# Kernel optimization log

Hardware: AMD Instinct MI355X
Metric: run time of the kernel (lower is better)

Reference implementation:

```python
import jax, jax.numpy as jnp
import numpy as np

N = 50000   # nodes (cells)
E = 800000  # directed edges
D = 512     # input/output feature dim (genes)
H = D // 64 # bottleneck dim = 8
LN_EPS = 1e-5


def setup_inputs() -> dict:
    key = jax.random.key(0)
    ks = jax.random.split(key, 6)
    x = jax.random.normal(ks[0], (N, D), dtype=jnp.float32)
    edge_index = jax.random.randint(ks[1], (2, E), 0, N, dtype=jnp.int64)
    size_factors = jax.random.uniform(ks[2], (N, 1), dtype=jnp.float32) + 0.5
    s1 = float(1.0 / np.sqrt(D))
    W1 = jax.random.uniform(ks[3], (D, H), jnp.float32, -s1, s1)
    b1 = jnp.zeros((H,), jnp.float32)
    gamma = jnp.ones((H,), jnp.float32)
    beta = jnp.zeros((H,), jnp.float32)
    s2 = float(1.0 / np.sqrt(H))
    W2 = jax.random.uniform(ks[4], (H, D), jnp.float32, -s2, s2)
    b2 = jnp.zeros((D,), jnp.float32)
    return {"x": x, "size_factors": size_factors, "W1": W1, "b1": b1,
            "gamma": gamma, "beta": beta, "W2": W2, "b2": b2,
            "edge_index": edge_index}


def _gcn_conv(x, W, b, src, dst, norm):
    # PyG GCNConv: linear transform, then sym-normalized scatter-add aggregation.
    h = x @ W                                   # [N, out]
    msg = h[src] * norm[:, None]                # [E+N, out] gather + scale
    out = jax.ops.segment_sum(msg, dst, num_segments=N)  # scatter-add
    return out + b


def reference(x, size_factors, W1, b1, gamma, beta, W2, b2, edge_index):
    loops = jnp.arange(N, dtype=edge_index.dtype)
    src = jnp.concatenate([edge_index[0], loops])  # add self-loops
    dst = jnp.concatenate([edge_index[1], loops])
    deg = jax.ops.segment_sum(jnp.ones_like(src, dtype=x.dtype), dst,
                              num_segments=N)       # deg >= 1 via self-loops
    dinv = jax.lax.rsqrt(deg)
    norm = dinv[src] * dinv[dst]                    # [E+N]

    h = _gcn_conv(x, W1, b1, src, dst, norm)        # [N, H]
    mu = jnp.mean(h, axis=-1, keepdims=True)
    var = jnp.var(h, axis=-1, keepdims=True)
    h = (h - mu) * jax.lax.rsqrt(var + LN_EPS) * gamma + beta
    h = jax.nn.relu(h)
    # dropout p=0.0 -> identity
    out = jax.nn.relu(_gcn_conv(h, W2, b2, src, dst, norm))  # [N, D]
    return out * size_factors
```

## Files before the change

kernel.cpp:

```cpp
#include <hip/hip_runtime.h>

#define NN 50000
#define EE 800000
#define DD 512
#define HH 8
#define BA 160
#define CHUNK 5000
#define NBIN 196
#define BCAP 4608
#define GBLK 782
#define NTILE 3125
#define AGBLK 1563
#define SCANT 192

typedef short bf16x8 __attribute__((ext_vector_type(8)));
typedef float f32x4 __attribute__((ext_vector_type(4)));

union U16 { uint4 u; bf16x8 v; unsigned short h[8]; };

__device__ __forceinline__ unsigned short f2bf(float f) {
    union { float f; unsigned int i; } c; c.f = f;
    unsigned int i = c.i;
    i += 0x7fffu + ((i >> 16) & 1u);
    return (unsigned short)(i >> 16);
}

__global__ __launch_bounds__(256) void k_gemm1_hist(const float4* __restrict__ x4,
                                                    const float* __restrict__ W1,
                                                    const int* __restrict__ dst,
                                                    float* __restrict__ t1,
                                                    int* __restrict__ blockhist) {
    __shared__ int smem[4096];
    int t = threadIdx.x;
    if (blockIdx.x >= GBLK) {
        int blk = blockIdx.x - GBLK;
        int* h = smem;
        h[t] = 0; __syncthreads();
        int base = blk * CHUNK;
#pragma unroll
        for (int it = 0; it < 20; ++it) {
            int i = it * 256 + t;
            if (i < CHUNK) atomicAdd(&h[dst[base + i] >> 8], 1);
        }
        __syncthreads();
        blockhist[blk * 256 + t] = h[t];
        return;
    }
    unsigned short* sbf = (unsigned short*)smem;
    for (int i = t; i < 16 * 64 * 8; i += 256) {
        int lane = (i >> 3) & 63, j = i & 7;
        int n = lane & 15;
        int k = (i >> 9) * 32 + ((lane >> 4) * 8) + j;
        sbf[i] = (n < HH) ? f2bf(W1[k * HH + n]) : (unsigned short)0;
    }
    __syncthreads();
    int wave = t >> 6, lane = t & 63;
    int tile = blockIdx.x * 4 + wave;
    if (tile >= NTILE) return;
    int node0 = tile * 16;
    int m = lane & 15, q = lane >> 4;
    const float4* xrow = x4 + (size_t)(node0 + m) * (DD / 4) + q * 2;
    const uint4* bfrag = (const uint4*)sbf;
    f32x4 acc = {0.f, 0.f, 0.f, 0.f};

    float4 bufA[8], bufB[8];
#define LOADG(buf, g)                                                      \
    _Pragma("unroll")                                                      \
    for (int s = 0; s < 4; ++s) {                                          \
        buf[2 * s]     = xrow[((g) * 4 + s) * 8];                          \
        buf[2 * s + 1] = xrow[((g) * 4 + s) * 8 + 1];                      \
    }
#define MFMAG(buf, g)                                                      \
    _Pragma("unroll")                                                      \
    for (int s = 0; s < 4; ++s) {                                          \
        U16 a, b;                                                          \
        float4 u0 = buf[2 * s], u1 = buf[2 * s + 1];                       \
        a.h[0] = f2bf(u0.x); a.h[1] = f2bf(u0.y);                          \
        a.h[2] = f2bf(u0.z); a.h[3] = f2bf(u0.w);                          \
        a.h[4] = f2bf(u1.x); a.h[5] = f2bf(u1.y);                          \
        a.h[6] = f2bf(u1.z); a.h[7] = f2bf(u1.w);                          \
        b.u = bfrag[((g) * 4 + s) * 64 + lane];                            \
        acc = __builtin_amdgcn_mfma_f32_16x16x32_bf16(a.v, b.v, acc, 0, 0, 0); \
    }
    LOADG(bufA, 0)
    LOADG(bufB, 1)
    MFMAG(bufA, 0)
    LOADG(bufA, 2)
    MFMAG(bufB, 1)
    LOADG(bufB, 3)
    MFMAG(bufA, 2)
    MFMAG(bufB, 3)
#undef LOADG
#undef MFMAG
    if (m < HH) {
        int base = (node0 + q * 4) * HH + m;
        t1[base]          = acc[0];
        t1[base + HH]     = acc[1];
        t1[base + 2 * HH] = acc[2];
        t1[base + 3 * HH] = acc[3];
    }
}

__global__ __launch_bounds__(SCANT) void k_scan_a(int* __restrict__ blockhist,
                                                  int* __restrict__ binTotal) {
    __shared__ int s[SCANT];
    int bin = blockIdx.x, t = threadIdx.x;
    int v = (t < BA) ? blockhist[t * 256 + bin] : 0;
    s[t] = v; __syncthreads();
    for (int off = 1; off < SCANT; off <<= 1) {
        int x = (t >= off) ? s[t - off] : 0;
        __syncthreads();
        if (t >= off) s[t] += x;
        __syncthreads();
    }
    if (t < BA) blockhist[t * 256 + bin] = s[t] - v;
    if (t == SCANT - 1) binTotal[bin] = s[t];
}

__global__ __launch_bounds__(256) void k_scan_b(const int* __restrict__ binTotal,
                                                int* __restrict__ binBase,
                                                int* __restrict__ row) {
    __shared__ int s[256];
    int t = threadIdx.x;
    int v = binTotal[t];
    s[t] = v; __syncthreads();
    for (int off = 1; off < 256; off <<= 1) {
        int x = (t >= off) ? s[t - off] : 0;
        __syncthreads();
        if (t >= off) s[t] += x;
        __syncthreads();
    }
    binBase[t] = s[t] - v;
    if (t == 255) { binBase[256] = s[255]; row[NN] = s[255]; }
}

__global__ __launch_bounds__(256) void k_scatter(const int* __restrict__ eidx,
                                                 const int* __restrict__ blockhist,
                                                 const int* __restrict__ binBase,
                                                 int* __restrict__ bucket) {
    __shared__ int cur[256];
    int t = threadIdx.x, blk = blockIdx.x;
    cur[t] = binBase[t] + blockhist[blk * 256 + t]; __syncthreads();
    int base = blk * CHUNK;
#pragma unroll
    for (int it = 0; it < 20; ++it) {
        int i = it * 256 + t;
        if (i < CHUNK) {
            int s = eidx[base + i], d = eidx[EE + base + i];
            int pos = atomicAdd(&cur[d >> 8], 1);
            bucket[pos] = (s << 8) | (d & 255);
        }
    }
}

__global__ __launch_bounds__(256) void k_build(const int* __restrict__ bucket,
                                               const int* __restrict__ binBase,
                                               int* __restrict__ row,
                                               int* __restrict__ adj,
                                               float* __restrict__ dinvA,
                                               float* __restrict__ t1) {
    __shared__ int smem[2 * BCAP + 768];
    int t = threadIdx.x;
    int bin = blockIdx.x;
    int n0 = bin << 8;
    int segStart = binBase[bin];
    int count = binBase[bin + 1] - segStart;
    if (count > BCAP) count = BCAP;
    int* lds_in  = smem;
    int* lds_out = smem + BCAP;
    int* cnt     = smem + 2 * BCAP;
    int* off     = smem + 2 * BCAP + 256;
    int* cur2    = smem + 2 * BCAP + 512;
    cnt[t] = 0; __syncthreads();
    for (int i = t; i < count; i += 256) {
        int p = bucket[segStart + i];
        lds_in[i] = p;
        atomicAdd(&cnt[p & 255], 1);
    }
    __syncthreads();
    off[t] = cnt[t]; __syncthreads();
    for (int o = 1; o < 256; o <<= 1) {
        int x = (t >= o) ? off[t - o] : 0;
        __syncthreads();
        if (t >= o) off[t] += x;
        __syncthreads();
    }
    int excl = off[t] - cnt[t];
    cur2[t] = excl;
    int n = n0 + t;
    if (n < NN) {
        row[n] = segStart + excl;
        float dv = rsqrtf((float)cnt[t] + 1.0f);
        dinvA[n] = dv;
        float4* tp = (float4*)(t1 + (size_t)n * HH);
        float4 a = tp[0], b = tp[1];
        a.x *= dv; a.y *= dv; a.z *= dv; a.w *= dv;
        b.x *= dv; b.y *= dv; b.z *= dv; b.w *= dv;
        tp[0] = a; tp[1] = b;
    }
    __syncthreads();
    for (int i = t; i < count; i += 256) {
        int p = lds_in[i];
        int pos = atomicAdd(&cur2[p & 255], 1);
        lds_out[pos] = p >> 8;
    }
    __syncthreads();
    for (int i = t; i < count; i += 256)
        adj[segStart + i] = lds_out[i];
}

__global__ __launch_bounds__(256) void k_agg1(const float* __restrict__ t1,
                                              const int* __restrict__ row,
                                              const int* __restrict__ adj,
                                              const float* __restrict__ dinvA,
                                              const float* __restrict__ b1,
                                              const float* __restrict__ gma,
                                              const float* __restrict__ bta,
                                              float* __restrict__ h2) {
    int gid = blockIdx.x * 256 + threadIdx.x;
    int n = gid >> 3, f = gid & 7;
    if (n >= NN) return;
    int beg = row[n], end = row[n + 1];
    float dv = dinvA[n];
    float acc = t1[(size_t)n * HH + f];
    int i = beg;
    for (; i < end && (i & 3); ++i)
        acc += t1[(size_t)adj[i] * HH + f];
    const int4* a4 = (const int4*)adj;
    for (; i + 8 <= end; i += 8) {
        int4 e0 = a4[i >> 2], e1 = a4[(i >> 2) + 1];
        float v0 = t1[(size_t)e0.x * HH + f], v1 = t1[(size_t)e0.y * HH + f];
        float v2 = t1[(size_t)e0.z * HH + f], v3 = t1[(size_t)e0.w * HH + f];
        float v4 = t1[(size_t)e1.x * HH + f], v5 = t1[(size_t)e1.y * HH + f];
        float v6 = t1[(size_t)e1.z * HH + f], v7 = t1[(size_t)e1.w * HH + f];
        acc += ((v0 + v1) + (v2 + v3)) + ((v4 + v5) + (v6 + v7));
    }
    if (i + 4 <= end) {
        int4 e0 = a4[i >> 2];
        float v0 = t1[(size_t)e0.x * HH + f], v1 = t1[(size_t)e0.y * HH + f];
        float v2 = t1[(size_t)e0.z * HH + f], v3 = t1[(size_t)e0.w * HH + f];
        acc += (v0 + v1) + (v2 + v3);
        i += 4;
    }
    for (; i < end; ++i)
        acc += t1[(size_t)adj[i] * HH + f];
    acc = acc * dv + b1[f];
    float s = acc;
    s += __shfl_xor(s, 1); s += __shfl_xor(s, 2); s += __shfl_xor(s, 4);
    float mu = s * 0.125f;
    float dx = acc - mu;
    float sq = dx * dx;
    sq += __shfl_xor(sq, 1); sq += __shfl_xor(sq, 2); sq += __shfl_xor(sq, 4);
    float rs = rsqrtf(sq * 0.125f + 1e-5f);
    h2[(size_t)n * HH + f] = fmaxf(dx * rs * gma[f] + bta[f], 0.f) * dv;
}

__global__ __launch_bounds__(256) void k_agg2_gemm2(const float* __restrict__ h2,
                                                    const int* __restrict__ row,
                                                    const int* __restrict__ adj,
                                                    const float* __restrict__ dinvA,
                                                    const float* __restrict__ W2,
                                                    const float* __restrict__ b2,
                                                    const float* __restrict__ sf,
                                                    float* __restrict__ out) {
    __shared__ float sA[32 * 8];
    int tid = threadIdx.x;
    int c = tid & 63, g = tid >> 6, d0 = c * 8;
    float w[8][8];
#pragma unroll
    for (int k = 0; k < 8; ++k) {
        float4 u0 = *(const float4*)(W2 + k * DD + d0);
        float4 u1 = *(const float4*)(W2 + k * DD + d0 + 4);
        w[k][0] = u0.x; w[k][1] = u0.y; w[k][2] = u0.z; w[k][3] = u0.w;
        w[k][4] = u1.x; w[k][5] = u1.y; w[k][6] = u1.z; w[k][7] = u1.w;
    }
    float bb[8];
    {
        float4 u0 = *(const float4*)(b2 + d0);
        float4 u1 = *(const float4*)(b2 + d0 + 4);
        bb[0] = u0.x; bb[1] = u0.y; bb[2] = u0.z; bb[3] = u0.w;
        bb[4] = u1.x; bb[5] = u1.y; bb[6] = u1.z; bb[7] = u1.w;
    }
    int nl = tid >> 3, f = tid & 7;
    int n = blockIdx.x * 32 + nl;
    if (n < NN) {
        int beg = row[n], end = row[n + 1];
        float dv = dinvA[n];
        float acc = h2[(size_t)n * HH + f];
        int i = beg;
        for (; i < end && (i & 3); ++i)
            acc += h2[(size_t)adj[i] * HH + f];
        const int4* a4 = (const int4*)adj;
        for (; i + 8 <= end; i += 8) {
            int4 e0 = a4[i >> 2], e1 = a4[(i >> 2) + 1];
            float v0 = h2[(size_t)e0.x * HH + f], v1 = h2[(size_t)e0.y * HH + f];
            float v2 = h2[(size_t)e0.z * HH + f], v3 = h2[(size_t)e0.w * HH + f];
            float v4 = h2[(size_t)e1.x * HH + f], v5 = h2[(size_t)e1.y * HH + f];
            float v6 = h2[(size_t)e1.z * HH + f], v7 = h2[(size_t)e1.w * HH + f];
            acc += ((v0 + v1) + (v2 + v3)) + ((v4 + v5) + (v6 + v7));
        }
        if (i + 4 <= end) {
            int4 e0 = a4[i >> 2];
            float v0 = h2[(size_t)e0.x * HH + f], v1 = h2[(size_t)e0.y * HH + f];
            float v2 = h2[(size_t)e0.z * HH + f], v3 = h2[(size_t)e0.w * HH + f];
            acc += (v0 + v1) + (v2 + v3);
            i += 4;
        }
        for (; i < end; ++i)
            acc += h2[(size_t)adj[i] * HH + f];
        sA[nl * 8 + f] = acc * dv;
    }
    __syncthreads();
#pragma unroll
    for (int i = 0; i < 8; ++i) {
        int rrow = i * 4 + g;
        int n2 = blockIdx.x * 32 + rrow;
        if (n2 < NN) {
            float a[8];
#pragma unroll
            for (int j = 0; j < 8; ++j) a[j] = sA[rrow * 8 + j];
            float s = sf[n2];
            float acc[8];
#pragma unroll
            for (int j = 0; j < 8; ++j) acc[j] = bb[j];
#pragma unroll
            for (int k = 0; k < 8; ++k)
#pragma unroll
                for (int j = 0; j < 8; ++j) acc[j] += a[k] * w[k][j];
            float4 o0 = make_float4(fmaxf(acc[0], 0.f) * s, fmaxf(acc[1], 0.f) * s,
                                    fmaxf(acc[2], 0.f) * s, fmaxf(acc[3], 0.f) * s);
            float4 o1 = make_float4(fmaxf(acc[4], 0.f) * s, fmaxf(acc[5], 0.f) * s,
                                    fmaxf(acc[6], 0.f) * s, fmaxf(acc[7], 0.f) * s);
            float4* op = (float4*)(out + (size_t)n2 * DD + d0);
            op[0] = o0;
            op[1] = o1;
        }
    }
}

extern "C" void kernel_launch(void* const* d_in, const int* in_sizes, int n_in,
                              void* d_out, int out_size, void* d_ws, size_t ws_size,
                              hipStream_t stream) {
    (void)in_sizes; (void)n_in; (void)out_size; (void)ws_size;
    const float* x   = (const float*)d_in[0];
    const float* sf  = (const float*)d_in[1];
    const float* W1  = (const float*)d_in[2];
    const float* b1  = (const float*)d_in[3];
    const float* gma = (const float*)d_in[4];
    const float* bta = (const float*)d_in[5];
    const float* W2  = (const float*)d_in[6];
    const float* b2  = (const float*)d_in[7];
    const int* eidx  = (const int*)d_in[8];
    float* out = (float*)d_out;

    char* ws = (char*)d_ws;
    int*   blockhist = (int*)(ws + 0);
    int*   binBase   = (int*)(ws + 262144);
    int*   binTotal  = (int*)(ws + 262144 + 2048);
    int*   row       = (int*)(ws + (1 << 20));
    float* dinvA     = (float*)(ws + 2 * (1 << 20));
    float* t1        = (float*)(ws + 3 * (1 << 20));
    float* h2        = (float*)(ws + 5 * (1 << 20));
    int*   adj       = (int*)(ws + 7 * (1 << 20));
    int*   bucket    = (int*)(ws + 11 * (1 << 20));

    k_gemm1_hist<<<GBLK + BA, 256, 0, stream>>>((const float4*)x, W1, eidx + EE,
                                                t1, blockhist);
    k_scan_a<<<256, SCANT, 0, stream>>>(blockhist, binTotal);
    k_scan_b<<<1, 256, 0, stream>>>(binTotal, binBase, row);
    k_scatter<<<BA, 256, 0, stream>>>(eidx, blockhist, binBase, bucket);
    k_build<<<NBIN, 256, 0, stream>>>(bucket, binBase, row, adj, dinvA, t1);
    k_agg1<<<AGBLK, 256, 0, stream>>>(t1, row, adj, dinvA, b1, gma, bta, h2);
    k_agg2_gemm2<<<AGBLK, 256, 0, stream>>>(h2, row, adj, dinvA, W2, b2, sf, out);
}
```

Before: 270.9 us.

## Replace binned two-level CSR build with global-atomic degree count and fill

Swaps the bucketed CSR construction (per-block histograms, two scans, bucket scatter, LDS-local sort) for a simpler scheme: global atomic degree counting, a two-kernel prefix scan over nodes, and a fill kernel that places each edge with a global atomicAdd on a per-node cursor. The aim is to remove the bucket pass and the heavier LDS build kernel, cutting one round trip of edge data. In exchange it relies on scattered global atomics, and the neighbour order within each row becomes nondeterministic, which can change float summation order. It also adds a memset launch.

New measurement: 316.6 us. +16.9%, slower.

```diff
diff --git a/kernel.cpp b/kernel.cpp
--- a/kernel.cpp
+++ b/kernel.cpp
@@ -4,14 +4,12 @@
 #define EE 800000
 #define DD 512
 #define HH 8
-#define BA 160
-#define CHUNK 5000
-#define NBIN 196
-#define BCAP 4608
 #define GBLK 782
+#define DBLK 391
 #define NTILE 3125
 #define AGBLK 1563
-#define SCANT 192
+#define SB 196
+#define NPAD 50176
 
 typedef short bf16x8 __attribute__((ext_vector_type(8)));
 typedef float f32x4 __attribute__((ext_vector_type(4)));
@@ -25,25 +23,20 @@
     return (unsigned short)(i >> 16);
 }
 
-__global__ __launch_bounds__(256) void k_gemm1_hist(const float4* __restrict__ x4,
-                                                    const float* __restrict__ W1,
-                                                    const int* __restrict__ dst,
-                                                    float* __restrict__ t1,
-                                                    int* __restrict__ blockhist) {
+__global__ __launch_bounds__(256) void k_gemm1_deg(const float4* __restrict__ x4,
+                                                   const float* __restrict__ W1,
+                                                   const int* __restrict__ dst,
+                                                   float* __restrict__ t1,
+                                                   int* __restrict__ deg) {
     __shared__ int smem[4096];
     int t = threadIdx.x;
     if (blockIdx.x >= GBLK) {
-        int blk = blockIdx.x - GBLK;
-        int* h = smem;
-        h[t] = 0; __syncthreads();
-        int base = blk * CHUNK;
-#pragma unroll
-        for (int it = 0; it < 20; ++it) {
-            int i = it * 256 + t;
-            if (i < CHUNK) atomicAdd(&h[dst[base + i] >> 8], 1);
+        int base = (blockIdx.x - GBLK) * 2048;
+#pragma unroll
+        for (int it = 0; it < 8; ++it) {
+            int i = base + it * 256 + t;
+            if (i < EE) atomicAdd(&deg[dst[i]], 1);
         }
-        __syncthreads();
-        blockhist[blk * 256 + t] = h[t];
         return;
     }
     unsigned short* sbf = (unsigned short*)smem;
@@ -101,28 +94,13 @@
     }
 }
 
-__global__ __launch_bounds__(SCANT) void k_scan_a(int* __restrict__ blockhist,
-                                                  int* __restrict__ binTotal) {
-    __shared__ int s[SCANT];
-    int bin = blockIdx.x, t = threadIdx.x;
-    int v = (t < BA) ? blockhist[t * 256 + bin] : 0;
-    s[t] = v; __syncthreads();
-    for (int off = 1; off < SCANT; off <<= 1) {
-        int x = (t >= off) ? s[t - off] : 0;
-        __syncthreads();
-        if (t >= off) s[t] += x;
-        __syncthreads();
-    }
-    if (t < BA) blockhist[t * 256 + bin] = s[t] - v;
-    if (t == SCANT - 1) binTotal[bin] = s[t];
-}
-
-__global__ __launch_bounds__(256) void k_scan_b(const int* __restrict__ binTotal,
-                                                int* __restrict__ binBase,
-                                                int* __restrict__ row) {
+__global__ __launch_bounds__(256) void k_scanA(const int* __restrict__ deg,
+                                               int* __restrict__ dlocal,
+                                               int* __restrict__ bsum) {
     __shared__ int s[256];
-    int t = threadIdx.x;
-    int v = binTotal[t];
+    int b = blockIdx.x, t = threadIdx.x;
+    int n = b * 256 + t;
+    int v = deg[n];
     s[t] = v; __syncthreads();
     for (int off = 1; off < 256; off <<= 1) {
         int x = (t >= off) ? s[t - off] : 0;
@@ -130,83 +108,51 @@
         if (t >= off) s[t] += x;
         __syncthreads();
     }
-    binBase[t] = s[t] - v;
-    if (t == 255) { binBase[256] = s[255]; row[NN] = s[255]; }
-}
-
-__global__ __launch_bounds__(256) void k_scatter(const int* __restrict__ eidx,
-                                                 const int* __restrict__ blockhist,
-                                                 const int* __restrict__ binBase,
-                                                 int* __restrict__ bucket) {
-    __shared__ int cur[256];
-    int t = threadIdx.x, blk = blockIdx.x;
-    cur[t] = binBase[t] + blockhist[blk * 256 + t]; __syncthreads();
-    int base = blk * CHUNK;
-#pragma unroll
-    for (int it = 0; it < 20; ++it) {
-        int i = it * 256 + t;
-        if (i < CHUNK) {
-            int s = eidx[base + i], d = eidx[EE + base + i];
-            int pos = atomicAdd(&cur[d >> 8], 1);
-            bucket[pos] = (s << 8) | (d & 255);
-        }
-    }
-}
-
-__global__ __launch_bounds__(256) void k_build(const int* __restrict__ bucket,
-                                               const int* __restrict__ binBase,
+    dlocal[n] = s[t] - v;
+    if (t == 255) bsum[b] = s[255];
+}
+
+__global__ __launch_bounds__(256) void k_scanB(const int* __restrict__ deg,
+                                               const int* __restrict__ dlocal,
+                                               const int* __restrict__ bsum,
+                                               float* __restrict__ t1,
                                                int* __restrict__ row,
-                                               int* __restrict__ adj,
-                                               float* __restrict__ dinvA,
-                                               float* __restrict__ t1) {
-    __shared__ int smem[2 * BCAP + 768];
-    int t = threadIdx.x;
-    int bin = blockIdx.x;
-    int n0 = bin << 8;
-    int segStart = binBase[bin];
-    int count = binBase[bin + 1] - segStart;
-    if (count > BCAP) count = BCAP;
-    int* lds_in  = smem;
-    int* lds_out = smem + BCAP;
-    int* cnt     = smem + 2 * BCAP;
-    int* off     = smem + 2 * BCAP + 256;
-    int* cur2    = smem + 2 * BCAP + 512;
-    cnt[t] = 0; __syncthreads();
-    for (int i = t; i < count; i += 256) {
-        int p = bucket[segStart + i];
-        lds_in[i] = p;
-        atomicAdd(&cnt[p & 255], 1);
-    }
+                                               int* __restrict__ cur,
+                                               float* __restrict__ dinvA) {
+    __shared__ int s[256];
+    int b = blockIdx.x, t = threadIdx.x;
+    s[t] = (t < SB) ? bsum[t] : 0;
     __syncthreads();
-    off[t] = cnt[t]; __syncthreads();
-    for (int o = 1; o < 256; o <<= 1) {
-        int x = (t >= o) ? off[t - o] : 0;
+    for (int off = 1; off < 256; off <<= 1) {
+        int x = (t >= off) ? s[t - off] : 0;
         __syncthreads();
-        if (t >= o) off[t] += x;
+        if (t >= off) s[t] += x;
         __syncthreads();
     }
-    int excl = off[t] - cnt[t];
-    cur2[t] = excl;
-    int n = n0 + t;
+    int base = s[b] - bsum[b];
+    int n = b * 256 + t;
     if (n < NN) {
-        row[n] = segStart + excl;
-        float dv = rsqrtf((float)cnt[t] + 1.0f);
+        int r = base + dlocal[n];
+        row[n] = r;
+        cur[n] = r;
+        float dv = rsqrtf((float)deg[n] + 1.0f);
         dinvA[n] = dv;
         float4* tp = (float4*)(t1 + (size_t)n * HH);
-        float4 a = tp[0], b = tp[1];
+        float4 a = tp[0], c = tp[1];
         a.x *= dv; a.y *= dv; a.z *= dv; a.w *= dv;
-        b.x *= dv; b.y *= dv; b.z *= dv; b.w *= dv;
-        tp[0] = a; tp[1] = b;
-    }
-    __syncthreads();
-    for (int i = t; i < count; i += 256) {
-        int p = lds_in[i];
-        int pos = atomicAdd(&cur2[p & 255], 1);
-        lds_out[pos] = p >> 8;
-    }
-    __syncthreads();
-    for (int i = t; i < count; i += 256)
-        adj[segStart + i] = lds_out[i];
+        c.x *= dv; c.y *= dv; c.z *= dv; c.w *= dv;
+        tp[0] = a; tp[1] = c;
+    }
+    if (b == 0 && t == 0) row[NN] = EE;
+}
+
+__global__ __launch_bounds__(256) void k_fill(const int* __restrict__ eidx,
+                                              int* __restrict__ cur,
+                                              int* __restrict__ adj) {
+    int i = blockIdx.x * 256 + threadIdx.x;
+    int s = eidx[i], d = eidx[EE + i];
+    int pos = atomicAdd(&cur[d], 1);
+    adj[pos] = s;
 }
 
 __global__ __launch_bounds__(256) void k_agg1(const float* __restrict__ t1,
@@ -354,22 +300,22 @@
     float* out = (float*)d_out;
 
     char* ws = (char*)d_ws;
-    int*   blockhist = (int*)(ws + 0);
-    int*   binBase   = (int*)(ws + 262144);
-    int*   binTotal  = (int*)(ws + 262144 + 2048);
-    int*   row       = (int*)(ws + (1 << 20));
-    float* dinvA     = (float*)(ws + 2 * (1 << 20));
-    float* t1        = (float*)(ws + 3 * (1 << 20));
-    float* h2        = (float*)(ws + 5 * (1 << 20));
-    int*   adj       = (int*)(ws + 7 * (1 << 20));
-    int*   bucket    = (int*)(ws + 11 * (1 << 20));
-
-    k_gemm1_hist<<<GBLK + BA, 256, 0, stream>>>((const float4*)x, W1, eidx + EE,
-                                                t1, blockhist);
-    k_scan_a<<<256, SCANT, 0, stream>>>(blockhist, binTotal);
-    k_scan_b<<<1, 256, 0, stream>>>(binTotal, binBase, row);
-    k_scatter<<<BA, 256, 0, stream>>>(eidx, blockhist, binBase, bucket);
-    k_build<<<NBIN, 256, 0, stream>>>(bucket, binBase, row, adj, dinvA, t1);
+    int*   deg    = (int*)(ws + 0);
+    int*   dlocal = (int*)(ws + 0x40000);
+    int*   bsum   = (int*)(ws + 0x80000);
+    int*   row    = (int*)(ws + (1 << 20));
+    int*   cur    = (int*)(ws + 0x180000);
+    float* dinvA  = (float*)(ws + 2 * (1 << 20));
+    float* t1     = (float*)(ws + 3 * (1 << 20));
+    float* h2     = (float*)(ws + 5 * (1 << 20));
+    int*   adj    = (int*)(ws + 7 * (1 << 20));
+
+    hipMemsetAsync(deg, 0, NPAD * sizeof(int), stream);
+    k_gemm1_deg<<<GBLK + DBLK, 256, 0, stream>>>((const float4*)x, W1, eidx + EE,
+                                                 t1, deg);
+    k_scanA<<<SB, 256, 0, stream>>>(deg, dlocal, bsum);
+    k_scanB<<<SB, 256, 0, stream>>>(deg, dlocal, bsum, t1, row, cur, dinvA);
+    k_fill<<<NTILE, 256, 0, stream>>>(eidx, cur, adj);
     k_agg1<<<AGBLK, 256, 0, stream>>>(t1, row, adj, dinvA, b1, gma, bta, h2);
     k_agg2_gemm2<<<AGBLK, 256, 0, stream>>>(h2, row, adj, dinvA, W2, b2, sf, out);
 }
```

## Pad CSR rows to multiples of four with a zero sentinel node

Applied to the files above, without the earlier changes.

Each node's adjacency list is padded to a multiple of 4 and aligned, and the padding slots point at a sentinel row N whose features are zeroed in t1 and h2. The aggregation loops then use only aligned int4 loads, with no scalar head or tail loops, and read separate begin/end arrays. This removes divergent scalar edge iterations in both aggregation kernels. The cost is extra gathers of the zero row, slightly more LDS in the build kernel, and a larger adjacency array.

Result: no change. 266.6 us (-1.6%).

```diff
diff --git a/kernel.cpp b/kernel.cpp
--- a/kernel.cpp
+++ b/kernel.cpp
@@ -8,6 +8,7 @@
 #define CHUNK 5000
 #define NBIN 196
 #define BCAP 4608
+#define BPAD 5632
 #define GBLK 782
 #define NTILE 3125
 #define AGBLK 1563
@@ -119,7 +120,7 @@
 
 __global__ __launch_bounds__(256) void k_scan_b(const int* __restrict__ binTotal,
                                                 int* __restrict__ binBase,
-                                                int* __restrict__ row) {
+                                                float* __restrict__ t1) {
     __shared__ int s[256];
     int t = threadIdx.x;
     int v = binTotal[t];
@@ -131,7 +132,8 @@
         __syncthreads();
     }
     binBase[t] = s[t] - v;
-    if (t == 255) { binBase[256] = s[255]; row[NN] = s[255]; }
+    if (t == 255) binBase[256] = s[255];
+    if (t < HH) t1[(size_t)NN * HH + t] = 0.f;
 }
 
 __global__ __launch_bounds__(256) void k_scatter(const int* __restrict__ eidx,
@@ -155,11 +157,12 @@
 
 __global__ __launch_bounds__(256) void k_build(const int* __restrict__ bucket,
                                                const int* __restrict__ binBase,
-                                               int* __restrict__ row,
+                                               int* __restrict__ beg,
+                                               int* __restrict__ endp,
                                                int* __restrict__ adj,
                                                float* __restrict__ dinvA,
                                                float* __restrict__ t1) {
-    __shared__ int smem[2 * BCAP + 768];
+    __shared__ int smem[BCAP + BPAD + 768];
     int t = threadIdx.x;
     int bin = blockIdx.x;
     int n0 = bin << 8;
@@ -168,9 +171,9 @@
     if (count > BCAP) count = BCAP;
     int* lds_in  = smem;
     int* lds_out = smem + BCAP;
-    int* cnt     = smem + 2 * BCAP;
-    int* off     = smem + 2 * BCAP + 256;
-    int* cur2    = smem + 2 * BCAP + 512;
+    int* cnt     = smem + BCAP + BPAD;
+    int* off     = smem + BCAP + BPAD + 256;
+    int* cur2    = smem + BCAP + BPAD + 512;
     cnt[t] = 0; __syncthreads();
     for (int i = t; i < count; i += 256) {
         int p = bucket[segStart + i];
@@ -178,18 +181,21 @@
         atomicAdd(&cnt[p & 255], 1);
     }
     __syncthreads();
-    off[t] = cnt[t]; __syncthreads();
+    int pcnt = (cnt[t] + 3) & ~3;
+    off[t] = pcnt; __syncthreads();
     for (int o = 1; o < 256; o <<= 1) {
         int x = (t >= o) ? off[t - o] : 0;
         __syncthreads();
         if (t >= o) off[t] += x;
         __syncthreads();
     }
-    int excl = off[t] - cnt[t];
-    cur2[t] = excl;
+    int pexcl = off[t] - pcnt;
+    cur2[t] = pexcl;
+    int pbase = ((segStart + 3) & ~3) + bin * 1024;
     int n = n0 + t;
     if (n < NN) {
-        row[n] = segStart + excl;
+        beg[n]  = pbase + pexcl;
+        endp[n] = pbase + pexcl + pcnt;
         float dv = rsqrtf((float)cnt[t] + 1.0f);
         dinvA[n] = dv;
         float4* tp = (float4*)(t1 + (size_t)n * HH);
@@ -199,35 +205,39 @@
         tp[0] = a; tp[1] = b;
     }
     __syncthreads();
+    int paddedCount = off[255];
+    for (int i = t; i < paddedCount; i += 256)
+        lds_out[i] = NN;
+    __syncthreads();
     for (int i = t; i < count; i += 256) {
         int p = lds_in[i];
         int pos = atomicAdd(&cur2[p & 255], 1);
         lds_out[pos] = p >> 8;
     }
     __syncthreads();
-    for (int i = t; i < count; i += 256)
-        adj[segStart + i] = lds_out[i];
+    for (int i = t; i < paddedCount; i += 256)
+        adj[pbase + i] = lds_out[i];
 }
 
 __global__ __launch_bounds__(256) void k_agg1(const float* __restrict__ t1,
-                                              const int* __restrict__ row,
-                                              const int* __restrict__ adj,
+                                              const int* __restrict__ beg,
+                                              const int* __restrict__ endp,
                                               const float* __restrict__ dinvA,
                                               const float* __restrict__ b1,
                                               const float* __restrict__ gma,
                                               const float* __restrict__ bta,
+                                              const int* __restrict__ adj,
                                               float* __restrict__ h2) {
+    if (blockIdx.x == 0 && threadIdx.x < HH)
+        h2[(size_t)NN * HH + threadIdx.x] = 0.f;
     int gid = blockIdx.x * 256 + threadIdx.x;
     int n = gid >> 3, f = gid & 7;
     if (n >= NN) return;
-    int beg = row[n], end = row[n + 1];
+    int i = beg[n], e = endp[n];
     float dv = dinvA[n];
     float acc = t1[(size_t)n * HH + f];
-    int i = beg;
-    for (; i < end && (i & 3); ++i)
-        acc += t1[(size_t)adj[i] * HH + f];
     const int4* a4 = (const int4*)adj;
-    for (; i + 8 <= end; i += 8) {
+    for (; i + 8 <= e; i += 8) {
         int4 e0 = a4[i >> 2], e1 = a4[(i >> 2) + 1];
         float v0 = t1[(size_t)e0.x * HH + f], v1 = t1[(size_t)e0.y * HH + f];
         float v2 = t1[(size_t)e0.z * HH + f], v3 = t1[(size_t)e0.w * HH + f];
@@ -235,15 +245,12 @@
         float v6 = t1[(size_t)e1.z * HH + f], v7 = t1[(size_t)e1.w * HH + f];
         acc += ((v0 + v1) + (v2 + v3)) + ((v4 + v5) + (v6 + v7));
     }
-    if (i + 4 <= end) {
+    if (i < e) {
         int4 e0 = a4[i >> 2];
         float v0 = t1[(size_t)e0.x * HH + f], v1 = t1[(size_t)e0.y * HH + f];
         float v2 = t1[(size_t)e0.z * HH + f], v3 = t1[(size_t)e0.w * HH + f];
         acc += (v0 + v1) + (v2 + v3);
-        i += 4;
-    }
-    for (; i < end; ++i)
-        acc += t1[(size_t)adj[i] * HH + f];
+    }
     acc = acc * dv + b1[f];
     float s = acc;
     s += __shfl_xor(s, 1); s += __shfl_xor(s, 2); s += __shfl_xor(s, 4);
@@ -256,12 +263,13 @@
 }
 
 __global__ __launch_bounds__(256) void k_agg2_gemm2(const float* __restrict__ h2,
-                                                    const int* __restrict__ row,
-                                                    const int* __restrict__ adj,
+                                                    const int* __restrict__ beg,
+                                                    const int* __restrict__ endp,
                                                     const float* __restrict__ dinvA,
                                                     const float* __restrict__ W2,
                                                     const float* __restrict__ b2,
                                                     const float* __restrict__ sf,
+                                                    const int* __restrict__ adj,
                                                     float* __restrict__ out) {
     __shared__ float sA[32 * 8];
     int tid = threadIdx.x;
@@ -284,14 +292,11 @@
     int nl = tid >> 3, f = tid & 7;
     int n = blockIdx.x * 32 + nl;
     if (n < NN) {
-        int beg = row[n], end = row[n + 1];
+        int i = beg[n], e = endp[n];
         float dv = dinvA[n];
         float acc = h2[(size_t)n * HH + f];
-        int i = beg;
-        for (; i < end && (i & 3); ++i)
-            acc += h2[(size_t)adj[i] * HH + f];
         const int4* a4 = (const int4*)adj;
-        for (; i + 8 <= end; i += 8) {
+        for (; i + 8 <= e; i += 8) {
             int4 e0 = a4[i >> 2], e1 = a4[(i >> 2) + 1];
             float v0 = h2[(size_t)e0.x * HH + f], v1 = h2[(size_t)e0.y * HH + f];
             float v2 = h2[(size_t)e0.z * HH + f], v3 = h2[(size_t)e0.w * HH + f];
@@ -299,15 +304,12 @@
             float v6 = h2[(size_t)e1.z * HH + f], v7 = h2[(size_t)e1.w * HH + f];
             acc += ((v0 + v1) + (v2 + v3)) + ((v4 + v5) + (v6 + v7));
         }
-        if (i + 4 <= end) {
+        if (i < e) {
             int4 e0 = a4[i >> 2];
             float v0 = h2[(size_t)e0.x * HH + f], v1 = h2[(size_t)e0.y * HH + f];
             float v2 = h2[(size_t)e0.z * HH + f], v3 = h2[(size_t)e0.w * HH + f];
             acc += (v0 + v1) + (v2 + v3);
-            i += 4;
-        }
-        for (; i < end; ++i)
-            acc += h2[(size_t)adj[i] * HH + f];
+        }
         sA[nl * 8 + f] = acc * dv;
     }
     __syncthreads();
@@ -355,21 +357,23 @@
 
     char* ws = (char*)d_ws;
     int*   blockhist = (int*)(ws + 0);
-    int*   binBase   = (int*)(ws + 262144);
-    int*   binTotal  = (int*)(ws + 262144 + 2048);
-    int*   row       = (int*)(ws + (1 << 20));
-    float* dinvA     = (float*)(ws + 2 * (1 << 20));
-    float* t1        = (float*)(ws + 3 * (1 << 20));
-    float* h2        = (float*)(ws + 5 * (1 << 20));
-    int*   adj       = (int*)(ws + 7 * (1 << 20));
-    int*   bucket    = (int*)(ws + 11 * (1 << 20));
+    int*   binBase   = (int*)(ws + 0x40000);
+    int*   binTotal  = (int*)(ws + 0x41000);
+    int*   beg       = (int*)(ws + 0x100000);
+    int*   endp      = (int*)(ws + 0x140000);
+    float* dinvA     = (float*)(ws + 0x200000);
+    float* t1        = (float*)(ws + 0x300000);
+    float* h2        = (float*)(ws + 0x500000);
+    int*   adj       = (int*)(ws + 0x700000);
+    int*   bucket    = (int*)(ws + 0xB00000);
 
     k_gemm1_hist<<<GBLK + BA, 256, 0, stream>>>((const float4*)x, W1, eidx + EE,
                                                 t1, blockhist);
     k_scan_a<<<256, SCANT, 0, stream>>>(blockhist, binTotal);
-    k_scan_b<<<1, 256, 0, stream>>>(binTotal, binBase, row);
+    k_scan_b<<<1, 256, 0, stream>>>(binTotal, binBase, t1);
     k_scatter<<<BA, 256, 0, stream>>>(eidx, blockhist, binBase, bucket);
-    k_build<<<NBIN, 256, 0, stream>>>(bucket, binBase, row, adj, dinvA, t1);
-    k_agg1<<<AGBLK, 256, 0, stream>>>(t1, row, adj, dinvA, b1, gma, bta, h2);
-    k_agg2_gemm2<<<AGBLK, 256, 0, stream>>>(h2, row, adj, dinvA, W2, b2, sf, out);
-}
+    k_build<<<NBIN, 256, 0, stream>>>(bucket, binBase, beg, endp, adj, dinvA, t1);
+    k_agg1<<<AGBLK, 256, 0, stream>>>(t1, beg, endp, dinvA, b1, gma, bta, adj, h2);
+    k_agg2_gemm2<<<AGBLK, 256, 0, stream>>>(h2, beg, endp, dinvA, W2, b2, sf, adj,
+                                            out);
+}
```
